# Optimization experiments

Measured on AMD Instinct MI355X. Metric: run time of the kernel, lower is better.

The kernel has to match this reference:

```python
import jax, jax.numpy as jnp
import numpy as np

B, S, D, H, F = 4, 1024, 1024, 16, 4096
DH = D // H
EPS = 1e-5


def _ln(x, g, b):
    mu = jnp.mean(x, axis=-1, keepdims=True)
    var = jnp.mean((x - mu) ** 2, axis=-1, keepdims=True)
    return (x - mu) * jax.lax.rsqrt(var + EPS) * g + b


def _mha(q_in, k_in, v_in, mask, wq, bq, wk, bk, wv, bv, wo, bo):
    b, sq, d = q_in.shape
    sk = k_in.shape[1]
    Q = (q_in @ wq + bq).reshape(b, sq, H, DH).transpose(0, 2, 1, 3)  # [B,H,Sq,dh]
    K = (k_in @ wk + bk).reshape(b, sk, H, DH).transpose(0, 2, 1, 3)
    V = (v_in @ wv + bv).reshape(b, sk, H, DH).transpose(0, 2, 1, 3)
    scores = jnp.einsum('bhqd,bhkd->bhqk', Q, K) / jnp.sqrt(jnp.asarray(DH, Q.dtype))
    if mask is not None:
        scores = jnp.where(mask[:, None] == 0, jnp.asarray(-1e9, scores.dtype), scores)
    w = jax.nn.softmax(scores, axis=-1)
    ctx = jnp.einsum('bhqk,bhkd->bhqd', w, V).transpose(0, 2, 1, 3).reshape(b, sq, d)
    return ctx @ wo + bo


def setup_inputs() -> dict:
    key = jax.random.key(0)
    ks = jax.random.split(key, 20)
    s = 0.02
    inp = {
        'x': jax.random.normal(ks[0], (B, S, D), jnp.float32),
        'src_x': jax.random.normal(ks[1], (B, S, D), jnp.float32),
        # causal self-attention mask (1 = keep), cross mask all ones
        'mask': jnp.broadcast_to(jnp.tril(jnp.ones((S, S), jnp.int32)), (B, S, S)),
        'src_mask': jnp.ones((B, S, S), jnp.int32),
        'ln1_g': jnp.ones((D,), jnp.float32), 'ln1_b': jnp.zeros((D,), jnp.float32),
        'ln2_g': jnp.ones((D,), jnp.float32), 'ln2_b': jnp.zeros((D,), jnp.float32),
        'ln3_g': jnp.ones((D,), jnp.float32), 'ln3_b': jnp.zeros((D,), jnp.float32),
    }
    names = ['sa_wq', 'sa_wk', 'sa_wv', 'sa_wo', 'ca_wq', 'ca_wk', 'ca_wv', 'ca_wo']
    for i, n in enumerate(names):
        inp[n] = jax.random.normal(ks[2 + i], (D, D), jnp.float32) * s
        inp[n.replace('w', 'b')] = jnp.zeros((D,), jnp.float32)
    inp['ff_w1'] = jax.random.normal(ks[10], (D, F), jnp.float32) * s
    inp['ff_b1'] = jnp.zeros((F,), jnp.float32)
    inp['ff_w2'] = jax.random.normal(ks[11], (F, D), jnp.float32) * s
    inp['ff_b2'] = jnp.zeros((D,), jnp.float32)
    return inp


def reference(x, mask, src_x, src_mask,
              ln1_g, ln1_b, ln2_g, ln2_b, ln3_g, ln3_b,
              sa_wq, sa_bq, sa_wk, sa_bk, sa_wv, sa_bv, sa_wo, sa_bo,
              ca_wq, ca_bq, ca_wk, ca_bk, ca_wv, ca_bv, ca_wo, ca_bo,
              ff_w1, ff_b1, ff_w2, ff_b2):
    # pre-layer-norm decoder layer (dropout = 0 / eval mode)
    h = _ln(x, ln1_g, ln1_b)
    x = x + _mha(h, h, h, mask, sa_wq, sa_bq, sa_wk, sa_bk, sa_wv, sa_bv, sa_wo, sa_bo)
    h = _ln(x, ln2_g, ln2_b)
    x = x + _mha(h, src_x, src_x, src_mask, ca_wq, ca_bq, ca_wk, ca_bk, ca_wv, ca_bv, ca_wo, ca_bo)
    h = _ln(x, ln3_g, ln3_b)
    x = x + (jax.nn.relu(h @ ff_w1 + ff_b1) @ ff_w2 + ff_b2)
    return x
```

## Files before the change

kernel.cpp:

```cpp
#include <hip/hip_runtime.h>
#include <hip/hip_bf16.h>

#define B_ 4
#define S_ 1024
#define D_ 1024
#define H_ 16
#define DH_ 64
#define F_ 4096

typedef unsigned short u16;
typedef unsigned int u32;
typedef __attribute__((ext_vector_type(8))) short bf16x8;
typedef __attribute__((ext_vector_type(4))) float f32x4;

__device__ __forceinline__ float bf2f(u16 u) {
    return __uint_as_float(((u32)u) << 16);
}
__device__ __forceinline__ u16 f2bf(float f) {
    __hip_bfloat16 h = __float2bfloat16(f);
    return *reinterpret_cast<u16*>(&h);
}

typedef __attribute__((address_space(1))) const u32 gu32;
typedef __attribute__((address_space(3))) u32 lu32;
__device__ __forceinline__ void gl_lds16(const void* g, void* l) {
    __builtin_amdgcn_global_load_lds((gu32*)g, (lu32*)l, 16, 0, 0);
}

__global__ __launch_bounds__(256) void cvt1_kernel(const float* __restrict__ s,
                                                   u16* __restrict__ d) {
    int i = (blockIdx.x * 256 + threadIdx.x) * 4;
    float4 v = *(const float4*)(s + i);
    u16 o0 = f2bf(v.x), o1 = f2bf(v.y), o2 = f2bf(v.z), o3 = f2bf(v.w);
    d[i] = o0; d[i+1] = o1; d[i+2] = o2; d[i+3] = o3;
}

__device__ __forceinline__ void trcvt_body(const float* __restrict__ src,
                                           u16* __restrict__ dst, int K, int N,
                                           int n0, int k0) {
    __shared__ u16 tile[64][65];
    int t = threadIdx.x;
    int c = t & 63, r4 = t >> 6;
#pragma unroll
    for (int i = 0; i < 16; i++) {
        int r = i * 4 + r4;
        tile[c][r] = f2bf(src[(size_t)(k0 + r) * N + n0 + c]);
    }
    __syncthreads();
#pragma unroll
    for (int i = 0; i < 16; i++) {
        int rr = i * 4 + r4;
        dst[(size_t)(n0 + rr) * K + k0 + c] = tile[rr][c];
    }
}

__global__ __launch_bounds__(256) void trcvt_kernel(const float* __restrict__ src,
                                                    u16* __restrict__ dst,
                                                    int K, int N) {
    trcvt_body(src, dst, K, N, blockIdx.x * 64, blockIdx.y * 64);
}

struct TP { const float* src[8]; u16* dst[8]; };
__global__ __launch_bounds__(256) void trcvt8_kernel(TP tp) {
    trcvt_body(tp.src[blockIdx.z], tp.dst[blockIdx.z], D_, D_,
               blockIdx.x * 64, blockIdx.y * 64);
}

__global__ __launch_bounds__(256) void mask_reduce_kernel(const int* __restrict__ mask,
                                                          unsigned char* __restrict__ bmask) {
    int t = threadIdx.x;
    int qb = blockIdx.x >> 4, kb = blockIdx.x & 15, b = blockIdx.y;
    bool all1 = true, any1 = false;
#pragma unroll
    for (int i = 0; i < 16; i++) {
        int e = t + i * 256;
        int r = e >> 6, c = e & 63;
        int v = mask[((size_t)(b * S_ + qb * 64 + r)) * S_ + kb * 64 + c];
        all1 = all1 && (v != 0);
        any1 = any1 || (v != 0);
    }
    unsigned long long ba = __ballot(all1), bn = __ballot(any1);
    __shared__ unsigned long long sa[4], sn[4];
    if ((t & 63) == 0) { sa[t >> 6] = ba; sn[t >> 6] = bn; }
    __syncthreads();
    if (t == 0) {
        bool A = ((sa[0] & sa[1] & sa[2] & sa[3]) == ~0ull);
        bool Y = ((sn[0] | sn[1] | sn[2] | sn[3]) != 0ull);
        bmask[b * 256 + blockIdx.x] = A ? 2 : (Y ? 1 : 0);
    }
}

template<bool COPY>
__global__ __launch_bounds__(256) void ln_kernel(const float* __restrict__ xin,
                                                 const float* __restrict__ g,
                                                 const float* __restrict__ bta,
                                                 float* xcur,
                                                 u16* __restrict__ hout) {
    int row = blockIdx.x;
    int t = threadIdx.x;
    size_t base = (size_t)row * D_;
    float v[4];
#pragma unroll
    for (int i = 0; i < 4; i++) v[i] = xin[base + t + i * 256];
    float s  = v[0] + v[1] + v[2] + v[3];
    float s2 = v[0]*v[0] + v[1]*v[1] + v[2]*v[2] + v[3]*v[3];
#pragma unroll
    for (int m = 1; m < 64; m <<= 1) {
        s  += __shfl_xor(s, m);
        s2 += __shfl_xor(s2, m);
    }
    __shared__ float red[8];
    int wave = t >> 6;
    if ((t & 63) == 0) { red[wave*2] = s; red[wave*2+1] = s2; }
    __syncthreads();
    float fs  = red[0] + red[2] + red[4] + red[6];
    float fs2 = red[1] + red[3] + red[5] + red[7];
    float mu  = fs * (1.0f / D_);
    float var = fs2 * (1.0f / D_) - mu * mu;
    float rs  = rsqrtf(var + 1e-5f);
#pragma unroll
    for (int i = 0; i < 4; i++) {
        int c = t + i * 256;
        float x = v[i];
        if (COPY) xcur[base + c] = x;
        hout[base + c] = f2bf((x - mu) * rs * g[c] + bta[c]);
    }
}

struct Bias3 { const float* b0; const float* b1; const float* b2; int n1; int n2; };

__device__ __forceinline__ float bias_at(const Bias3& bs, int c) {
    const float* p; int o;
    if (c < bs.n1)      { p = bs.b0; o = c; }
    else if (c < bs.n2) { p = bs.b1; o = c - bs.n1; }
    else                { p = bs.b2; o = c - bs.n2; }
    return p[o];
}

template<int BM, int BN, int OUT_MODE, bool BIAS_ROW>
__global__ __launch_bounds__(256) void gemm128_kernel(const u16* __restrict__ A,
                                                      const u16* __restrict__ Bt,
                                                      Bias3 bias,
                                                      const float* res,
                                                      void* out,
                                                      int M, int N, int K) {
    constexpr int MT = (BM == 64) ? 4 : (BN == 64 ? 2 : 4);
    constexpr int NT = (BN == 64) ? 4 : (BM == 64 ? 2 : 4);
    __shared__ u16 As[2][BM * 64];
    __shared__ u16 Bs[2][BN * 64];
    int t = threadIdx.x;
    int m0 = blockIdx.y * BM, n0 = blockIdx.x * BN;
    int w = t >> 6, lane = t & 63, quad = lane >> 4, l16 = lane & 15;
    int wm, wn;
    if (BM == 128 && BN == 128) { wm = (w >> 1) * 64; wn = (w & 1) * 64; }
    else if (BN == 64)          { wm = w * 32;        wn = 0; }
    else                        { wm = 0;             wn = w * 32; }

    f32x4 acc[MT][NT] = {};
    int sr = lane >> 3;
    int gc = ((lane & 7) ^ sr) * 8;
    int x7 = l16 & 7;
    const u16* gA = A + (size_t)m0 * K;
    const u16* gB = Bt + (size_t)n0 * K;

    auto stage = [&](int k0, int buf) {
#pragma unroll
        for (int j = w; j < BM / 8; j += 4)
            gl_lds16(gA + (size_t)(j * 8 + sr) * K + k0 + gc, &As[buf][j * 512]);
#pragma unroll
        for (int j = w; j < BN / 8; j += 4)
            gl_lds16(gB + (size_t)(j * 8 + sr) * K + k0 + gc, &Bs[buf][j * 512]);
    };

    stage(0, 0);
    int cur = 0;
    for (int k0 = 0; k0 < K; k0 += 64) {
        __syncthreads();
        if (k0 + 64 < K) stage(k0 + 64, cur ^ 1);

#pragma unroll
        for (int s = 0; s < 2; s++) {
            bf16x8 af[MT], bfr[NT];
            int cp = ((s * 4 + quad) ^ x7) * 8;
#pragma unroll
            for (int mt = 0; mt < MT; mt++)
                af[mt] = *(const bf16x8*)&As[cur][(wm + mt * 16 + l16) * 64 + cp];
#pragma unroll
            for (int nt = 0; nt < NT; nt++)
                bfr[nt] = *(const bf16x8*)&Bs[cur][(wn + nt * 16 + l16) * 64 + cp];
#pragma unroll
            for (int mt = 0; mt < MT; mt++)
#pragma unroll
                for (int nt = 0; nt < NT; nt++)
                    acc[mt][nt] = __builtin_amdgcn_mfma_f32_16x16x32_bf16(af[mt], bfr[nt], acc[mt][nt], 0, 0, 0);
        }
        cur ^= 1;
    }

#pragma unroll
    for (int nt = 0; nt < NT; nt++) {
        int col = n0 + wn + nt * 16 + l16;
        float bc = BIAS_ROW ? 0.f : bias_at(bias, col);
#pragma unroll
        for (int mt = 0; mt < MT; mt++) {
#pragma unroll
            for (int r = 0; r < 4; r++) {
                int row = m0 + wm + mt * 16 + quad * 4 + r;
                float v = acc[mt][nt][r] + (BIAS_ROW ? bias_at(bias, row) : bc);
                if (OUT_MODE == 1) v = fmaxf(v, 0.f);
                if (OUT_MODE == 2) {
                    v += res[(size_t)row * N + col];
                    ((float*)out)[(size_t)row * N + col] = v;
                } else {
                    ((u16*)out)[(size_t)row * N + col] = f2bf(v);
                }
            }
        }
    }
}

__global__ __launch_bounds__(256) void attn_kernel(const u16* __restrict__ Q, int ldq,
                                                   const u16* __restrict__ Kb, int ldk,
                                                   const u16* __restrict__ Vt,
                                                   const int* __restrict__ mask,
                                                   const unsigned char* __restrict__ bmask,
                                                   u16* __restrict__ ctx) {
    __shared__ u16 Ks[2][64 * 64];
    __shared__ u16 Vs[2][64 * 64];
    __shared__ u16 Ps[4][16 * 72];
    int t = threadIdx.x;
    int b = blockIdx.z, hh = blockIdx.y;
    int w = t >> 6, lane = t & 63, quad = lane >> 4, l16 = lane & 15;
    int hoff = hh * DH_;

    int qt[2] = { (int)blockIdx.x, 15 - (int)blockIdx.x };

    bf16x8 ones;
#pragma unroll
    for (int j = 0; j < 8; j++) ones[j] = (short)0x3F80;

    bf16x8 qf[2][2];
#pragma unroll
    for (int tt = 0; tt < 2; tt++) {
        int qrow = qt[tt] * 64 + w * 16 + l16;
#pragma unroll
        for (int kk = 0; kk < 2; kk++) {
            bf16x8 v = *(const bf16x8*)(Q + (size_t)(b * S_ + qrow) * ldq + hoff + kk * 32 + quad * 8);
#pragma unroll
            for (int j = 0; j < 8; j++)
                v[j] = (short)f2bf(bf2f((u16)v[j]) * 0.125f);
            qf[tt][kk] = v;
        }
    }

    f32x4 oacc[2][4] = {};
    f32x4 lacc[2] = {};

    unsigned nz[2], mx[2];
#pragma unroll
    for (int tt = 0; tt < 2; tt++) {
        nz[tt] = 0; mx[tt] = 0;
        for (int c = 0; c < 16; c++) {
            int v = bmask ? (int)bmask[(b * 16 + qt[tt]) * 16 + c] : 1;
            if (v)      nz[tt] |= 1u << c;
            if (v == 1) mx[tt] |= 1u << c;
        }
    }

    int sr = lane >> 3;
    int gc = ((lane & 7) ^ sr) * 8;

    auto stage = [&](int kb, int buf) {
        int k0 = kb * 64;
        for (int j = w; j < 8; j += 4) {
            gl_lds16(Kb + (size_t)(b * S_ + k0 + j * 8 + sr) * ldk + hoff + gc, &Ks[buf][j * 512]);
            gl_lds16(Vt + (size_t)(hoff + j * 8 + sr) * (B_ * S_) + b * S_ + k0 + gc, &Vs[buf][j * 512]);
        }
    };

    unsigned rem = nz[0] | nz[1];
    int cur = 0;
    int kb = rem ? __builtin_ctz(rem) : 16;
    if (kb < 16) stage(kb, 0);

    while (kb < 16) {
        rem &= rem - 1;
        int nkb = rem ? __builtin_ctz(rem) : 16;
        __syncthreads();
        if (nkb < 16) stage(nkb, cur ^ 1);
        int k0 = kb * 64;

#pragma unroll
        for (int tt = 0; tt < 2; tt++) {
            if (!((nz[tt] >> kb) & 1)) continue;
            bool mixed = (mx[tt] >> kb) & 1;

            float p[4][4];
#pragma unroll
            for (int nt = 0; nt < 4; nt++) {
                f32x4 sacc = {};
                int krow = nt * 16 + l16;
#pragma unroll
                for (int kk = 0; kk < 2; kk++) {
                    int cp = ((kk * 4 + quad) ^ (krow & 7)) * 8;
                    bf16x8 kf = *(const bf16x8*)&Ks[cur][krow * 64 + cp];
                    sacc = __builtin_amdgcn_mfma_f32_16x16x32_bf16(qf[tt][kk], kf, sacc, 0, 0, 0);
                }
                int kcol = k0 + nt * 16 + l16;
#pragma unroll
                for (int r = 0; r < 4; r++) {
                    float sv = sacc[r];
                    if (mixed) {
                        int qq = qt[tt] * 64 + w * 16 + quad * 4 + r;
                        if (mask[(size_t)(b * S_ + qq) * S_ + kcol] == 0) sv = -1e9f;
                    }
                    p[nt][r] = __expf(fminf(sv, 20.f));
                }
            }

#pragma unroll
            for (int nt = 0; nt < 4; nt++)
#pragma unroll
                for (int r = 0; r < 4; r++)
                    Ps[w][(quad * 4 + r) * 72 + nt * 16 + l16] = f2bf(p[nt][r]);

            bf16x8 pf[2];
#pragma unroll
            for (int kk = 0; kk < 2; kk++)
                pf[kk] = *(const bf16x8*)&Ps[w][l16 * 72 + kk * 32 + quad * 8];

            lacc[tt] = __builtin_amdgcn_mfma_f32_16x16x32_bf16(pf[0], ones, lacc[tt], 0, 0, 0);
            lacc[tt] = __builtin_amdgcn_mfma_f32_16x16x32_bf16(pf[1], ones, lacc[tt], 0, 0, 0);

#pragma unroll
            for (int dt = 0; dt < 4; dt++) {
                int vrow = dt * 16 + l16;
#pragma unroll
                for (int kk = 0; kk < 2; kk++) {
                    int cp = ((kk * 4 + quad) ^ (vrow & 7)) * 8;
                    bf16x8 vf = *(const bf16x8*)&Vs[cur][vrow * 64 + cp];
                    oacc[tt][dt] = __builtin_amdgcn_mfma_f32_16x16x32_bf16(pf[kk], vf, oacc[tt][dt], 0, 0, 0);
                }
            }
        }
        kb = nkb;
        cur ^= 1;
    }

#pragma unroll
    for (int tt = 0; tt < 2; tt++)
#pragma unroll
        for (int dt = 0; dt < 4; dt++)
#pragma unroll
            for (int r = 0; r < 4; r++) {
                int qq = qt[tt] * 64 + w * 16 + quad * 4 + r;
                float l = lacc[tt][r];
                float inv = l > 0.f ? 1.f / l : 0.f;
                ctx[(size_t)(b * S_ + qq) * D_ + hoff + dt * 16 + l16] = f2bf(oacc[tt][dt][r] * inv);
            }
}

extern "C" void kernel_launch(void* const* d_in, const int* in_sizes, int n_in,
                              void* d_out, int out_size, void* d_ws, size_t ws_size,
                              hipStream_t stream) {
    const float* x     = (const float*)d_in[0];
    const float* srcx  = (const float*)d_in[1];
    const int*   mask  = (const int*)d_in[2];
    const int*   smask = (const int*)d_in[3];
    const float* ln1g = (const float*)d_in[4],  *ln1b = (const float*)d_in[5];
    const float* ln2g = (const float*)d_in[6],  *ln2b = (const float*)d_in[7];
    const float* ln3g = (const float*)d_in[8],  *ln3b = (const float*)d_in[9];
    const float* sa_wq = (const float*)d_in[10], *sa_bq = (const float*)d_in[11];
    const float* sa_wk = (const float*)d_in[12], *sa_bk = (const float*)d_in[13];
    const float* sa_wv = (const float*)d_in[14], *sa_bv = (const float*)d_in[15];
    const float* sa_wo = (const float*)d_in[16], *sa_bo = (const float*)d_in[17];
    const float* ca_wq = (const float*)d_in[18], *ca_bq = (const float*)d_in[19];
    const float* ca_wk = (const float*)d_in[20], *ca_bk = (const float*)d_in[21];
    const float* ca_wv = (const float*)d_in[22], *ca_bv = (const float*)d_in[23];
    const float* ca_wo = (const float*)d_in[24], *ca_bo = (const float*)d_in[25];
    const float* ff_w1 = (const float*)d_in[26], *ff_b1 = (const float*)d_in[27];
    const float* ff_w2 = (const float*)d_in[28], *ff_b2 = (const float*)d_in[29];

    char* ws = (char*)d_ws;
    const size_t MB = 1ull << 20;
    const size_t DD = (size_t)D_ * D_;
    float* xcur = (float*)ws;
    u16* h     = (u16*)(ws + 16 * MB);
    u16* qk    = (u16*)(ws + 24 * MB);
    u16* qb    = (u16*)(ws + 24 * MB);
    u16* kbuf  = (u16*)(ws + 32 * MB);
    u16* vt    = (u16*)(ws + 40 * MB);
    u16* ctx   = (u16*)(ws + 48 * MB);
    u16* ff    = (u16*)(ws + 24 * MB);
    u16* sxb   = (u16*)(ws + 56 * MB);
    u16* wqk_s = (u16*)(ws + 64 * MB);
    u16* wv_s  = (u16*)(ws + 68 * MB);
    u16* wo_s  = (u16*)(ws + 70 * MB);
    u16* wq_c  = (u16*)(ws + 72 * MB);
    u16* wk_c  = (u16*)(ws + 74 * MB);
    u16* wv_c  = (u16*)(ws + 76 * MB);
    u16* wo_c  = (u16*)(ws + 78 * MB);
    u16* wff1  = (u16*)(ws + 80 * MB);
    u16* wff2  = (u16*)(ws + 88 * MB);
    unsigned char* bm_self = nullptr, *bm_cross = nullptr;
    if (ws_size >= 96 * MB + 8192) {
        bm_self  = (unsigned char*)(ws + ws_size - 8192);
        bm_cross = bm_self + 4096;
    }

    dim3 blk(256);

    TP tp = {{sa_wq, sa_wk, sa_wv, sa_wo, ca_wq, ca_wk, ca_wv, ca_wo},
             {wqk_s, wqk_s + DD, wv_s, wo_s, wq_c, wk_c, wv_c, wo_c}};
    trcvt8_kernel<<<dim3(16, 16, 8), blk, 0, stream>>>(tp);
    trcvt_kernel<<<dim3(F_ / 64, D_ / 64), blk, 0, stream>>>(ff_w1, wff1, D_, F_);
    trcvt_kernel<<<dim3(D_ / 64, F_ / 64), blk, 0, stream>>>(ff_w2, wff2, F_, D_);
    cvt1_kernel<<<B_ * S_ * D_ / 1024, blk, 0, stream>>>(srcx, sxb);
    if (bm_self) {
        mask_reduce_kernel<<<dim3(256, B_), blk, 0, stream>>>(mask, bm_self);
        mask_reduce_kernel<<<dim3(256, B_), blk, 0, stream>>>(smask, bm_cross);
    }

    Bias3 bqk = { sa_bq, sa_bk, sa_bk, 1024, 2048 };
    Bias3 bsv = { sa_bv, sa_bv, sa_bv, 1 << 30, 1 << 30 };
    Bias3 bso = { sa_bo, sa_bo, sa_bo, 1 << 30, 1 << 30 };
    Bias3 bcq = { ca_bq, ca_bq, ca_bq, 1 << 30, 1 << 30 };
    Bias3 bck = { ca_bk, ca_bk, ca_bk, 1 << 30, 1 << 30 };
    Bias3 bcv = { ca_bv, ca_bv, ca_bv, 1 << 30, 1 << 30 };
    Bias3 bco = { ca_bo, ca_bo, ca_bo, 1 << 30, 1 << 30 };
    Bias3 bf1 = { ff_b1, ff_b1, ff_b1, 1 << 30, 1 << 30 };
    Bias3 bf2 = { ff_b2, ff_b2, ff_b2, 1 << 30, 1 << 30 };

    ln_kernel<true><<<B_ * S_, blk, 0, stream>>>(x, ln1g, ln1b, xcur, h);
    gemm128_kernel<128,128,0,false><<<dim3(16, 32), blk, 0, stream>>>(h, wqk_s, bqk, nullptr, qk, 4096, 2048, 1024);
    gemm128_kernel<64,128,0,true><<<dim3(32, 16), blk, 0, stream>>>(wv_s, h, bsv, nullptr, vt, 1024, 4096, 1024);
    attn_kernel<<<dim3(8, H_, B_), blk, 0, stream>>>(qk, 2048, qk + 1024, 2048, vt, mask, bm_self, ctx);
    gemm128_kernel<128,64,2,false><<<dim3(16, 32), blk, 0, stream>>>(ctx, wo_s, bso, xcur, xcur, 4096, 1024, 1024);

    ln_kernel<false><<<B_ * S_, blk, 0, stream>>>(xcur, ln2g, ln2b, nullptr, h);
    gemm128_kernel<128,64,0,false><<<dim3(16, 32), blk, 0, stream>>>(h, wq_c, bcq, nullptr, qb, 4096, 1024, 1024);
    gemm128_kernel<128,64,0,false><<<dim3(16, 32), blk, 0, stream>>>(sxb, wk_c, bck, nullptr, kbuf, 4096, 1024, 1024);
    gemm128_kernel<64,128,0,true><<<dim3(32, 16), blk, 0, stream>>>(wv_c, sxb, bcv, nullptr, vt, 1024, 4096, 1024);
    attn_kernel<<<dim3(8, H_, B_), blk, 0, stream>>>(qb, 1024, kbuf, 1024, vt, smask, bm_cross, ctx);
    gemm128_kernel<128,64,2,false><<<dim3(16, 32), blk, 0, stream>>>(ctx, wo_c, bco, xcur, xcur, 4096, 1024, 1024);

    ln_kernel<false><<<B_ * S_, blk, 0, stream>>>(xcur, ln3g, ln3b, nullptr, h);
    gemm128_kernel<128,128,1,false><<<dim3(32, 32), blk, 0, stream>>>(h, wff1, bf1, nullptr, ff, 4096, 4096, 1024);
    gemm128_kernel<128,64,2,false><<<dim3(16, 32), blk, 0, stream>>>(ff, wff2, bf2, xcur, (float*)d_out, 4096, 1024, 4096);
}
```

Measured before the change: 590.6 us.

## Compute transposed scores to keep P in registers and stage 128-key super-tiles

The attention kernel now computes S^T by swapping the MFMA operands, so each lane holds probabilities in the layout the PV MFMA expects. This removes the per-wave LDS round trip for P, and the V fragments are gathered from two 4-element LDS reads instead. Key/value staging is grouped into 128-key super-tiles (two 64-key chunks per buffer), which halves the barrier count and doubles shared memory use to 64 KB. That larger footprint may reduce occupancy, and the split V reads add LDS instructions.

```diff
diff --git a/kernel.cpp b/kernel.cpp
--- a/kernel.cpp
+++ b/kernel.cpp
@@ -11,6 +11,7 @@
 typedef unsigned short u16;
 typedef unsigned int u32;
 typedef __attribute__((ext_vector_type(8))) short bf16x8;
+typedef __attribute__((ext_vector_type(4))) short bf16x4;
 typedef __attribute__((ext_vector_type(4))) float f32x4;
 
 __device__ __forceinline__ float bf2f(u16 u) {
@@ -225,9 +226,8 @@
                                                    const int* __restrict__ mask,
                                                    const unsigned char* __restrict__ bmask,
                                                    u16* __restrict__ ctx) {
-    __shared__ u16 Ks[2][64 * 64];
-    __shared__ u16 Vs[2][64 * 64];
-    __shared__ u16 Ps[4][16 * 72];
+    __shared__ u16 Ks[2][2][64 * 64];
+    __shared__ u16 Vs[2][2][64 * 64];
     int t = threadIdx.x;
     int b = blockIdx.z, hh = blockIdx.y;
     int w = t >> 6, lane = t & 63, quad = lane >> 4, l16 = lane & 15;
@@ -235,9 +235,9 @@
 
     int qt[2] = { (int)blockIdx.x, 15 - (int)blockIdx.x };
 
-    bf16x8 ones;
-#pragma unroll
-    for (int j = 0; j < 8; j++) ones[j] = (short)0x3F80;
+    bf16x8 ones8;
+#pragma unroll
+    for (int j = 0; j < 8; j++) ones8[j] = (short)0x3F80;
 
     bf16x8 qf[2][2];
 #pragma unroll
@@ -266,84 +266,97 @@
             if (v == 1) mx[tt] |= 1u << c;
         }
     }
+    unsigned nzU = nz[0] | nz[1];
+    unsigned remS = 0;
+    for (int s = 0; s < 8; s++) if ((nzU >> (2 * s)) & 3u) remS |= 1u << s;
 
     int sr = lane >> 3;
     int gc = ((lane & 7) ^ sr) * 8;
 
-    auto stage = [&](int kb, int buf) {
-        int k0 = kb * 64;
+    auto stage64 = [&](int c, int buf) {
+        int k0 = c * 64, c64 = c & 1;
         for (int j = w; j < 8; j += 4) {
-            gl_lds16(Kb + (size_t)(b * S_ + k0 + j * 8 + sr) * ldk + hoff + gc, &Ks[buf][j * 512]);
-            gl_lds16(Vt + (size_t)(hoff + j * 8 + sr) * (B_ * S_) + b * S_ + k0 + gc, &Vs[buf][j * 512]);
+            gl_lds16(Kb + (size_t)(b * S_ + k0 + j * 8 + sr) * ldk + hoff + gc, &Ks[buf][c64][j * 512]);
+            gl_lds16(Vt + (size_t)(hoff + j * 8 + sr) * (B_ * S_) + b * S_ + k0 + gc, &Vs[buf][c64][j * 512]);
         }
     };
-
-    unsigned rem = nz[0] | nz[1];
+    auto stageS = [&](int s, int buf) {
+        if ((nzU >> (2 * s)) & 1u)     stage64(2 * s, buf);
+        if ((nzU >> (2 * s + 1)) & 1u) stage64(2 * s + 1, buf);
+    };
+
     int cur = 0;
-    int kb = rem ? __builtin_ctz(rem) : 16;
-    if (kb < 16) stage(kb, 0);
-
-    while (kb < 16) {
-        rem &= rem - 1;
-        int nkb = rem ? __builtin_ctz(rem) : 16;
+    int s = remS ? __builtin_ctz(remS) : 8;
+    if (s < 8) stageS(s, 0);
+
+    while (s < 8) {
+        remS &= remS - 1;
+        int ns = remS ? __builtin_ctz(remS) : 8;
         __syncthreads();
-        if (nkb < 16) stage(nkb, cur ^ 1);
-        int k0 = kb * 64;
-
-#pragma unroll
-        for (int tt = 0; tt < 2; tt++) {
-            if (!((nz[tt] >> kb) & 1)) continue;
-            bool mixed = (mx[tt] >> kb) & 1;
-
-            float p[4][4];
-#pragma unroll
-            for (int nt = 0; nt < 4; nt++) {
-                f32x4 sacc = {};
-                int krow = nt * 16 + l16;
-#pragma unroll
-                for (int kk = 0; kk < 2; kk++) {
-                    int cp = ((kk * 4 + quad) ^ (krow & 7)) * 8;
-                    bf16x8 kf = *(const bf16x8*)&Ks[cur][krow * 64 + cp];
-                    sacc = __builtin_amdgcn_mfma_f32_16x16x32_bf16(qf[tt][kk], kf, sacc, 0, 0, 0);
+        if (ns < 8) stageS(ns, cur ^ 1);
+
+#pragma unroll
+        for (int c64 = 0; c64 < 2; c64++) {
+            int c = 2 * s + c64;
+            if (!((nzU >> c) & 1u)) continue;
+            int k0c = c * 64;
+            const u16* KsT = &Ks[cur][c64][0];
+            const u16* VsT = &Vs[cur][c64][0];
+
+#pragma unroll
+            for (int tt = 0; tt < 2; tt++) {
+                if (!((nz[tt] >> c) & 1u)) continue;
+                bool mixed = (mx[tt] >> c) & 1u;
+
+                float p[4][4];
+#pragma unroll
+                for (int nt = 0; nt < 4; nt++) {
+                    f32x4 sacc = {};
+                    int krow = nt * 16 + l16;
+#pragma unroll
+                    for (int kk = 0; kk < 2; kk++) {
+                        int cp = ((kk * 4 + quad) ^ (krow & 7)) * 8;
+                        bf16x8 kf = *(const bf16x8*)&KsT[krow * 64 + cp];
+                        sacc = __builtin_amdgcn_mfma_f32_16x16x32_bf16(kf, qf[tt][kk], sacc, 0, 0, 0);
+                    }
+#pragma unroll
+                    for (int r = 0; r < 4; r++) {
+                        float sv = sacc[r];
+                        if (mixed) {
+                            int qq = qt[tt] * 64 + w * 16 + l16;
+                            int kc = k0c + nt * 16 + quad * 4 + r;
+                            if (mask[(size_t)(b * S_ + qq) * S_ + kc] == 0) sv = -1e9f;
+                        }
+                        p[nt][r] = __expf(fminf(sv, 20.f));
+                    }
                 }
-                int kcol = k0 + nt * 16 + l16;
-#pragma unroll
-                for (int r = 0; r < 4; r++) {
-                    float sv = sacc[r];
-                    if (mixed) {
-                        int qq = qt[tt] * 64 + w * 16 + quad * 4 + r;
-                        if (mask[(size_t)(b * S_ + qq) * S_ + kcol] == 0) sv = -1e9f;
+
+#pragma unroll
+                for (int mp = 0; mp < 2; mp++) {
+                    bf16x8 af;
+#pragma unroll
+                    for (int r = 0; r < 4; r++) {
+                        af[r]     = (short)f2bf(p[2 * mp][r]);
+                        af[4 + r] = (short)f2bf(p[2 * mp + 1][r]);
                     }
-                    p[nt][r] = __expf(fminf(sv, 20.f));
+                    lacc[tt] = __builtin_amdgcn_mfma_f32_16x16x32_bf16(af, ones8, lacc[tt], 0, 0, 0);
+#pragma unroll
+                    for (int dt = 0; dt < 4; dt++) {
+                        int vrow = dt * 16 + l16;
+                        int ch0 = ((2 * mp) * 2 + (quad >> 1)) ^ (vrow & 7);
+                        int ch1 = ((2 * mp + 1) * 2 + (quad >> 1)) ^ (vrow & 7);
+                        int off = (quad & 1) * 4;
+                        bf16x4 lo = *(const bf16x4*)&VsT[vrow * 64 + ch0 * 8 + off];
+                        bf16x4 hi = *(const bf16x4*)&VsT[vrow * 64 + ch1 * 8 + off];
+                        bf16x8 vf;
+#pragma unroll
+                        for (int j = 0; j < 4; j++) { vf[j] = lo[j]; vf[4 + j] = hi[j]; }
+                        oacc[tt][dt] = __builtin_amdgcn_mfma_f32_16x16x32_bf16(af, vf, oacc[tt][dt], 0, 0, 0);
+                    }
                 }
             }
-
-#pragma unroll
-            for (int nt = 0; nt < 4; nt++)
-#pragma unroll
-                for (int r = 0; r < 4; r++)
-                    Ps[w][(quad * 4 + r) * 72 + nt * 16 + l16] = f2bf(p[nt][r]);
-
-            bf16x8 pf[2];
-#pragma unroll
-            for (int kk = 0; kk < 2; kk++)
-                pf[kk] = *(const bf16x8*)&Ps[w][l16 * 72 + kk * 32 + quad * 8];
-
-            lacc[tt] = __builtin_amdgcn_mfma_f32_16x16x32_bf16(pf[0], ones, lacc[tt], 0, 0, 0);
-            lacc[tt] = __builtin_amdgcn_mfma_f32_16x16x32_bf16(pf[1], ones, lacc[tt], 0, 0, 0);
-
-#pragma unroll
-            for (int dt = 0; dt < 4; dt++) {
-                int vrow = dt * 16 + l16;
-#pragma unroll
-                for (int kk = 0; kk < 2; kk++) {
-                    int cp = ((kk * 4 + quad) ^ (vrow & 7)) * 8;
-                    bf16x8 vf = *(const bf16x8*)&Vs[cur][vrow * 64 + cp];
-                    oacc[tt][dt] = __builtin_amdgcn_mfma_f32_16x16x32_bf16(pf[kk], vf, oacc[tt][dt], 0, 0, 0);
-                }
-            }
-        }
-        kb = nkb;
+        }
+        s = ns;
         cur ^= 1;
     }
 
```

New measurement: 575.2 us. 1.03x faster.
